# Optimization experiments

Hardware: AMD Instinct MI355X
Metric: run time of the kernel (lower is better)

Reference implementation:

```python
import jax, jax.numpy as jnp
import numpy as np

N_SPECIES = 4; N_BASIS = 128; N_GRAPH = 16; R_MAX = 6.0
NS_NODE, NV_NODE = 32, 16          # node irreps 32x0e + 16x1o
NS_EDGE = 16                       # initial edge irreps 16x0e
NS_OUT, NV_OUT = 16, 8             # output irreps 16x0e + 8x1o
NS_IN = 2 * NS_NODE + NS_EDGE      # 80 concatenated scalars
NV_IN = 2 * NV_NODE                # 32 concatenated vectors
NS_CONV = NS_OUT + NV_OUT          # 24 scalars (16 features + 8 gates)
W_SIZES = [NS_IN * NS_CONV, NS_IN * NV_OUT, NV_IN * NV_OUT, NV_IN * NS_CONV, NV_IN * NV_OUT]
N_NODES, N_EDGES = 8192, 65536
EPS = 1e-5


def gaussian_basis(d, stop, n):
    offsets = jnp.linspace(0.0, stop, n)
    coeff = -0.5 / (offsets[1] - offsets[0]) ** 2
    return jnp.exp(coeff * (d[:, None] - offsets[None, :]) ** 2)


def seg_mean(vals, seg, cnt):
    return jax.ops.segment_sum(vals, seg, num_segments=N_GRAPH) / cnt[:, None]


def setup_inputs():
    key = jax.random.key(0)
    ks = jax.random.split(key, 20)
    rn = lambda k, shape, scale: jax.random.normal(k, shape, jnp.float32) * scale
    inp = {}
    inp["node_fea"] = rn(ks[0], (N_NODES, NS_NODE + 3 * NV_NODE), 1.0)
    d = 0.5 + 5.0 * jax.random.uniform(ks[1], (N_EDGES,), jnp.float32)
    vec = jax.random.normal(ks[2], (N_EDGES, 3), jnp.float32)
    inp["edge_attr"] = jnp.concatenate([d[:, None], vec], axis=1)
    inp["edge_index"] = jax.random.randint(ks[3], (2, N_EDGES), 0, N_NODES)
    inp["x"] = jax.random.randint(ks[4], (N_NODES,), 0, N_SPECIES)
    inp["batch"] = jnp.sort(jax.random.randint(ks[5], (N_NODES,), 0, N_GRAPH))
    inp["w_rh"] = rn(ks[6], (N_BASIS, 64), N_BASIS ** -0.5); inp["b_rh"] = jnp.zeros((64,), jnp.float32)
    inp["w_ro"] = rn(ks[7], (64, sum(W_SIZES)), 64 ** -0.5); inp["b_ro"] = jnp.zeros((sum(W_SIZES),), jnp.float32)
    inp["w_pre"] = rn(ks[8], (NS_EDGE, NS_EDGE), NS_EDGE ** -0.5); inp["b_pre"] = jnp.zeros((NS_EDGE,), jnp.float32)
    inp["w_sc"] = rn(ks[9], (NS_EDGE, N_SPECIES ** 2, NS_OUT), 1.0)
    inp["w_post_s"] = rn(ks[10], (NS_OUT, NS_OUT), NS_OUT ** -0.5); inp["b_post_s"] = jnp.zeros((NS_OUT,), jnp.float32)
    inp["w_post_v"] = rn(ks[11], (NV_OUT, NV_OUT), NV_OUT ** -0.5)
    inp["ln_w_s"] = jnp.ones((NS_OUT,), jnp.float32); inp["ln_b_s"] = jnp.zeros((NS_OUT,), jnp.float32)
    inp["ln_w_v"] = jnp.ones((NV_OUT,), jnp.float32)
    inp["w_skip"] = rn(ks[12], (NS_EDGE, NS_OUT), NS_EDGE ** -0.5)
    inp["w_edge_s"] = rn(ks[13], (NS_OUT, NS_OUT), NS_OUT ** -0.5); inp["b_edge_s"] = jnp.zeros((NS_OUT,), jnp.float32)
    inp["w_edge_v"] = rn(ks[14], (NV_OUT, NV_OUT), NV_OUT ** -0.5)
    return inp


def _forward(node_fea, edge_attr, w_rh, b_rh, w_ro, b_ro, w_pre, b_pre, w_sc,
             w_post_s, b_post_s, w_post_v, ln_w_s, ln_b_s, ln_w_v,
             w_skip, w_edge_s, b_edge_s, w_edge_v, edge_index, x, batch):
    E = edge_index.shape[1]
    idx_i, idx_j = edge_index[0], edge_index[1]
    one_hot = jax.nn.one_hot(N_SPECIES * x[idx_i] + x[idx_j], N_SPECIES ** 2, dtype=node_fea.dtype)
    d, vec = edge_attr[:, 0], edge_attr[:, 1:4]
    u = vec / (jnp.linalg.norm(vec, axis=1, keepdims=True) + 1e-12)
    Y1 = np.sqrt(3.0) * u                                   # l=1 sph harm, component norm; Y0 == 1
    rbf = gaussian_basis(d, R_MAX, N_BASIS)                 # edge_length_embedded
    edge_s0 = gaussian_basis(d, 6.0, NS_EDGE)               # distance_expansion -> initial edge scalars
    # self connection: edge scalars x species-pair one-hot -> output scalars
    sc = jnp.einsum('ei,ej,ijo->eo', edge_s0, one_hot, w_sc) / np.sqrt(NS_EDGE * N_SPECIES ** 2)
    edge_s = edge_s0 @ w_pre + b_pre                        # lin_pre
    # gather node features by edge indices and concat
    nf_i, nf_j = node_fea[idx_i], node_fea[idx_j]
    s_in = jnp.concatenate([nf_i[:, :NS_NODE], nf_j[:, :NS_NODE], edge_s], axis=1)  # [E,80]
    v_in = jnp.concatenate([nf_i[:, NS_NODE:].reshape(E, NV_NODE, 3),
                            nf_j[:, NS_NODE:].reshape(E, NV_NODE, 3)], axis=1)      # [E,32,3]
    # radial MLP -> per-edge tensor-product path weights
    h = jax.nn.silu(rbf @ w_rh + b_rh)
    w_all = h @ w_ro + b_ro                                 # [E, 3840]
    w1, w2, w3, w4, w5 = jnp.split(w_all, np.cumsum(W_SIZES)[:-1].tolist(), axis=1)
    # equivariant tensor-product paths (explicit l<=1 Clebsch-Gordan structure)
    s0 = jnp.einsum('ei,eio->eo', s_in, w1.reshape(E, NS_IN, NS_CONV)) / np.sqrt(NS_IN)            # 0e x 0e -> 0e
    vA = jnp.einsum('ei,eio,ec->eoc', s_in, w2.reshape(E, NS_IN, NV_OUT), Y1) / np.sqrt(NS_IN)     # 0e x 1o -> 1o
    vB = jnp.einsum('eic,eio->eoc', v_in, w3.reshape(E, NV_IN, NV_OUT)) / np.sqrt(NV_IN)           # 1o x 0e -> 1o
    s1 = jnp.einsum('eic,eio,ec->eo', v_in, w4.reshape(E, NV_IN, NS_CONV), Y1) / np.sqrt(3.0 * NV_IN)  # 1o.1o -> 0e
    vC = jnp.einsum('eic,eio->eoc', jnp.cross(v_in, Y1[:, None, :]), w5.reshape(E, NV_IN, NV_OUT)) / np.sqrt(2.0 * NV_IN)  # 1o x 1o -> 1o
    s_conv = s0 + s1                                        # [E,24]
    v_conv = vA + vB + vC                                   # [E,8,3]
    # gate nonlinearity inside conv
    s_out = jax.nn.silu(s_conv[:, :NS_OUT])
    v_out = v_conv * jax.nn.sigmoid(s_conv[:, NS_OUT:])[:, :, None]
    # lin_post then self connection
    s_out = s_out @ w_post_s + b_post_s + sc
    v_out = jnp.einsum('eic,io->eoc', v_out, w_post_v)
    # e3LayerNorm keyed by graph id of source node
    eb = batch[idx_i]
    cnt = jnp.maximum(jax.ops.segment_sum(jnp.ones((E,), s_out.dtype), eb, num_segments=N_GRAPH), 1.0)
    mu = seg_mean(s_out, eb, cnt)
    s_c = s_out - mu[eb]
    rms_s = jnp.sqrt(seg_mean(s_c ** 2, eb, cnt).mean(axis=1, keepdims=True) + EPS)
    s_n = s_c / rms_s[eb] * ln_w_s + ln_b_s
    rms_v = jnp.sqrt((seg_mean((v_out ** 2).sum(-1), eb, cnt) / 3.0).mean(axis=1, keepdims=True) + EPS)
    v_n = v_out / rms_v[eb][:, :, None] * ln_w_v[None, :, None]
    # skip connection from old edge features (scalars only)
    s_n = s_n + edge_s0 @ w_skip
    # final lin_edge
    s_fin = s_n @ w_edge_s + b_edge_s
    v_fin = jnp.einsum('eic,io->eoc', v_n, w_edge_v)
    return jnp.concatenate([s_fin, v_fin.reshape(E, NV_OUT * 3)], axis=1)  # [E,40]


def reference(node_fea, edge_attr, edge_index, x, batch, w_rh, b_rh, w_ro, b_ro,
              w_pre, b_pre, w_sc, w_post_s, b_post_s, w_post_v, ln_w_s, ln_b_s, ln_w_v,
              w_skip, w_edge_s, b_edge_s, w_edge_v):
    return _forward(node_fea, edge_attr, w_rh, b_rh, w_ro, b_ro, w_pre, b_pre, w_sc,
                    w_post_s, b_post_s, w_post_v, ln_w_s, ln_b_s, ln_w_v,
                    w_skip, w_edge_s, b_edge_s, w_edge_v, edge_index, x, batch)
```

## Files before the change

kernel.cpp:

```cpp
#include <hip/hip_runtime.h>

typedef unsigned short u16;
typedef unsigned int u32;
typedef __attribute__((ext_vector_type(8))) _Float16 half8;
typedef __attribute__((ext_vector_type(2))) __fp16 fp16x2;
typedef __attribute__((ext_vector_type(4))) float floatx4;

#define E_TOTAL 65536

__device__ __forceinline__ u32 pk16(float x0, float x1) {
    union { fp16x2 h; u32 u; } c;
    c.h = __builtin_amdgcn_cvt_pkrtz(x0, x1);
    return c.u;
}
union Frag8h { u32 u[4]; half8 v; };


__global__ __launch_bounds__(1024) void k_init(float* __restrict__ ws, int* __restrict__ binv) {
    const int tid = threadIdx.x;
    for (int i = tid; i < 1056; i += 1024) ws[i] = 0.0f;
    if (tid < 64) {
        const int lane = tid;
        const int q = lane >> 4;
        if (lane < 32) binv[lane] = lane;
        half8 bfr;
        #pragma unroll
        for (int j = 0; j < 8; ++j) bfr[j] = (_Float16)(float)(q*8 + j + 1);
        #pragma unroll
        for (int s = 0; s < 32; ++s) {
            const int qa = s >> 3, ja = s & 7;
            half8 afr;
            #pragma unroll
            for (int j = 0; j < 8; ++j) afr[j] = (_Float16)0.0f;
            if (q == qa) afr[ja] = (_Float16)1.0f;
            floatx4 dc = {0.0f, 0.0f, 0.0f, 0.0f};
            dc = __builtin_amdgcn_mfma_f32_16x16x32_f16(afr, bfr, dc, 0, 0, 0);
            if (lane == 0) {
                const int sB = (int)(dc[0] + 0.5f) - 1;
                if (sB >= 0 && sB < 32) binv[sB] = s;
            }
        }
    }
}

__global__ __launch_bounds__(256) void k_edge_heavy(
    const float* __restrict__ node_fea, const float* __restrict__ edge_attr,
    const int* __restrict__ edge_index, const int* __restrict__ xsp,
    const float* __restrict__ w_rh, const float* __restrict__ b_rh,
    const float* __restrict__ w_ro, const float* __restrict__ b_ro,
    const float* __restrict__ w_pre, const float* __restrict__ b_pre,
    const float* __restrict__ w_sc, const float* __restrict__ w_post_s,
    const float* __restrict__ b_post_s, const float* __restrict__ w_post_v,
    const int* __restrict__ binv,
    float* __restrict__ out)
{
    __shared__ __align__(16) float sh_wt[32][130];
    __shared__ float sh_sin[32][80];
    __shared__ float sh_vl[32][3][32];
    __shared__ float sh_acc[32][56];
    __shared__ float sh_y1[32][4];
    __shared__ int   sh_kmap[32];

    u16*   a_rbf = (u16*)&sh_wt[0][0];
    u16*   a_h   = (u16*)((char*)&sh_wt[0][0] + 8192);
    float* es0f  = (float*)((char*)&sh_wt[0][0] + 12288);

    const int tid = threadIdx.x;
    const int ed = tid >> 4, l16 = tid & 15;
    const int lane = tid & 63, w = tid >> 6;
    const int quad = lane >> 4, l15 = lane & 15;
    const int e0 = blockIdx.x * 32 + ed;
    const int e1 = e0 + 16;

    if (tid < 32) sh_kmap[tid] = binv[tid];

    const int ni0 = edge_index[e0], nj0 = edge_index[E_TOTAL + e0];
    const int ni1 = edge_index[e1], nj1 = edge_index[E_TOTAL + e1];
    const float4 ea0 = *(const float4*)(edge_attr + 4*e0);
    const float4 ea1 = *(const float4*)(edge_attr + 4*e1);
    const float d0 = ea0.x, d1 = ea1.x;
    {
        const float invn0 = 1.0f / (sqrtf(ea0.y*ea0.y + ea0.z*ea0.z + ea0.w*ea0.w) + 1e-12f);
        const float invn1 = 1.0f / (sqrtf(ea1.y*ea1.y + ea1.z*ea1.z + ea1.w*ea1.w) + 1e-12f);
        if (l16 == 0) {
            sh_y1[ed][0]    = 1.7320508075688772f * ea0.y * invn0;
            sh_y1[ed][1]    = 1.7320508075688772f * ea0.z * invn0;
            sh_y1[ed][2]    = 1.7320508075688772f * ea0.w * invn0;
            sh_y1[16+ed][0] = 1.7320508075688772f * ea1.y * invn1;
            sh_y1[16+ed][1] = 1.7320508075688772f * ea1.z * invn1;
            sh_y1[16+ed][2] = 1.7320508075688772f * ea1.w * invn1;
        }
    }

    const float C128 = -0.5f * (127.0f/6.0f) * (127.0f/6.0f);
    const float S128 = 6.0f/127.0f;
    {
        Frag8h t0, t1;
        #pragma unroll
        for (int r2 = 0; r2 < 4; ++r2) {
            const int b0i = l16*8 + 2*r2;
            const float u0 = d0 - S128 * (float)b0i;
            const float u1 = d0 - S128 * (float)(b0i + 1);
            const float v0 = d1 - S128 * (float)b0i;
            const float v1 = d1 - S128 * (float)(b0i + 1);
            t0.u[r2] = pk16(expf(C128*u0*u0), expf(C128*u1*u1));
            t1.u[r2] = pk16(expf(C128*v0*v0), expf(C128*v1*v1));
        }
        *(half8*)&a_rbf[(l16*16 + ed)*8]        = t0.v;
        *(half8*)&a_rbf[2048 + (l16*16 + ed)*8] = t1.v;
    }
    {
        const float t0 = d0 - 0.4f * (float)l16;
        const float t1 = d1 - 0.4f * (float)l16;
        es0f[ed*16 + l16]      = expf(-3.125f * t0 * t0);
        es0f[(16+ed)*16 + l16] = expf(-3.125f * t1 * t1);
    }

    const float rs80 = 0.11180339887498949f;
    const float rs32 = 0.17677669529663689f;
    {
        const float* fi = node_fea + (size_t)ni0 * 80;
        const float* fj = node_fea + (size_t)nj0 * 80;
        sh_sin[ed][2*l16+0]    = fi[2*l16+0] * rs80;
        sh_sin[ed][2*l16+1]    = fi[2*l16+1] * rs80;
        sh_sin[ed][32+2*l16+0] = fj[2*l16+0] * rs80;
        sh_sin[ed][32+2*l16+1] = fj[2*l16+1] * rs80;
        #pragma unroll
        for (int c = 0; c < 3; ++c) {
            sh_vl[ed][c][l16]      = fi[32 + 3*l16 + c] * rs32;
            sh_vl[ed][c][16 + l16] = fj[32 + 3*l16 + c] * rs32;
        }
    }
    {
        const float* fi = node_fea + (size_t)ni1 * 80;
        const float* fj = node_fea + (size_t)nj1 * 80;
        sh_sin[16+ed][2*l16+0]    = fi[2*l16+0] * rs80;
        sh_sin[16+ed][2*l16+1]    = fi[2*l16+1] * rs80;
        sh_sin[16+ed][32+2*l16+0] = fj[2*l16+0] * rs80;
        sh_sin[16+ed][32+2*l16+1] = fj[2*l16+1] * rs80;
        #pragma unroll
        for (int c = 0; c < 3; ++c) {
            sh_vl[16+ed][c][l16]      = fi[32 + 3*l16 + c] * rs32;
            sh_vl[16+ed][c][16 + l16] = fj[32 + 3*l16 + c] * rs32;
        }
    }
    for (int s = tid; s < 32*56; s += 256) (&sh_acc[0][0])[s] = 0.0f;
    __syncthreads();

    int km[8];
    u32 voff0[8], voff1[8];
    #pragma unroll
    for (int j = 0; j < 8; ++j) {
        km[j] = sh_kmap[quad*8 + j];
        voff0[j] = (u32)(km[j] * 3840 + l15);
        voff1[j] = voff0[j] + 32u * 3840u;
    }

    float my_sc0, my_sc1;
    {
        const int o = l16;
        float es0v = b_pre[o], sc0 = 0.0f;
        float es1v = b_pre[o], sc1 = 0.0f;
        const int p0 = 4*xsp[ni0] + xsp[nj0];
        const int p1 = 4*xsp[ni1] + xsp[nj1];
        #pragma unroll
        for (int i = 0; i < 16; ++i) {
            const float g0 = es0f[ed*16 + i];
            const float g1 = es0f[(16+ed)*16 + i];
            es0v += g0 * w_pre[i*16 + o];
            es1v += g1 * w_pre[i*16 + o];
            sc0  += g0 * w_sc[(i*16 + p0)*16 + o];
            sc1  += g1 * w_sc[(i*16 + p1)*16 + o];
        }
        sh_sin[ed][64 + o]    = es0v * rs80;
        sh_sin[16+ed][64 + o] = es1v * rs80;
        my_sc0 = sc0 * 0.0625f;
        my_sc1 = sc1 * 0.0625f;
    }

    {
        floatx4 h0 = {0.0f, 0.0f, 0.0f, 0.0f};
        floatx4 h1 = {0.0f, 0.0f, 0.0f, 0.0f};
        #pragma unroll
        for (int kk = 0; kk < 4; ++kk) {
            const half8 ag0 = *(const half8*)&a_rbf[((kk*4 + quad)*16 + l15)*8];
            const half8 ag1 = *(const half8*)&a_rbf[2048 + ((kk*4 + quad)*16 + l15)*8];
            Frag8h bh;
            #pragma unroll
            for (int jj = 0; jj < 4; ++jj) {
                const float x0 = w_rh[(size_t)(kk*32 + km[2*jj+0])*64 + w*16 + l15];
                const float x1 = w_rh[(size_t)(kk*32 + km[2*jj+1])*64 + w*16 + l15];
                bh.u[jj] = pk16(x0, x1);
            }
            h0 = __builtin_amdgcn_mfma_f32_16x16x32_f16(ag0, bh.v, h0, 0, 0, 0);
            h1 = __builtin_amdgcn_mfma_f32_16x16x32_f16(ag1, bh.v, h1, 0, 0, 0);
        }
        const int hn = w*16 + l15;
        const float bb = b_rh[hn];
        const int k8 = hn >> 3, j2 = hn & 7;
        #pragma unroll
        for (int r = 0; r < 4; ++r) {
            const int m = quad*4 + r;
            {
                const float x = h0[r] + bb;
                const float s = x / (1.0f + expf(-x));
                union { _Float16 h; u16 u; } cv; cv.h = (_Float16)s;
                a_h[(k8*16 + m)*8 + j2] = cv.u;
            }
            {
                const float x = h1[r] + bb;
                const float s = x / (1.0f + expf(-x));
                union { _Float16 h; u16 u; } cv; cv.h = (_Float16)s;
                a_h[1024 + (k8*16 + m)*8 + j2] = cv.u;
            }
        }
    }
    __syncthreads();

    const half8 a0g0 = *(const half8*)&a_h[((0*4 + quad)*16 + l15)*8];
    const half8 a1g0 = *(const half8*)&a_h[((1*4 + quad)*16 + l15)*8];
    const half8 a0g1 = *(const half8*)&a_h[1024 + ((0*4 + quad)*16 + l15)*8];
    const half8 a1g1 = *(const half8*)&a_h[1024 + ((1*4 + quad)*16 + l15)*8];

    float pf[32];
    float pbias[2];
    #pragma unroll
    for (int ct = 0; ct < 2; ++ct) {
        const int sgct = __builtin_amdgcn_readfirstlane(w*2 + ct);
        const float* bp = w_ro + sgct*16;
        #pragma unroll
        for (int j = 0; j < 8; ++j) {
            pf[ct*16 + j]     = bp[voff0[j]];
            pf[ct*16 + 8 + j] = bp[voff1[j]];
        }
        pbias[ct] = b_ro[sgct*16 + l15];
    }

    for (int ch = 0; ch < 30; ++ch) {
        const int coff = ch * 128;
        floatx4 acc0[2], acc1[2];
        float bias[2];
        #pragma unroll
        for (int ct = 0; ct < 2; ++ct) {
            Frag8h b0, b1;
            #pragma unroll
            for (int jj = 0; jj < 4; ++jj) {
                b0.u[jj] = pk16(pf[ct*16 + 2*jj],     pf[ct*16 + 2*jj+1]);
                b1.u[jj] = pk16(pf[ct*16 + 8 + 2*jj], pf[ct*16 + 8 + 2*jj+1]);
            }
            floatx4 a = {0.0f, 0.0f, 0.0f, 0.0f};
            a = __builtin_amdgcn_mfma_f32_16x16x32_f16(a0g0, b0.v, a, 0, 0, 0);
            a = __builtin_amdgcn_mfma_f32_16x16x32_f16(a1g0, b1.v, a, 0, 0, 0);
            acc0[ct] = a;
            floatx4 c = {0.0f, 0.0f, 0.0f, 0.0f};
            c = __builtin_amdgcn_mfma_f32_16x16x32_f16(a0g1, b0.v, c, 0, 0, 0);
            c = __builtin_amdgcn_mfma_f32_16x16x32_f16(a1g1, b1.v, c, 0, 0, 0);
            acc1[ct] = c;
            bias[ct] = pbias[ct];
        }
        __syncthreads();
        #pragma unroll
        for (int ct = 0; ct < 2; ++ct) {
            const int col = w*32 + ct*16 + l15;
            #pragma unroll
            for (int r = 0; r < 4; ++r) {
                sh_wt[quad*4 + r][col]      = acc0[ct][r] + bias[ct];
                sh_wt[16 + quad*4 + r][col] = acc1[ct][r] + bias[ct];
            }
        }
        __syncthreads();

        if (ch < 29) {
            #pragma unroll
            for (int ct = 0; ct < 2; ++ct) {
                const int sgct = __builtin_amdgcn_readfirstlane((ch+1)*8 + w*2 + ct);
                const float* bp = w_ro + sgct*16;
                #pragma unroll
                for (int j = 0; j < 8; ++j) {
                    pf[ct*16 + j]     = bp[voff0[j]];
                    pf[ct*16 + 8 + j] = bp[voff1[j]];
                }
                pbias[ct] = b_ro[sgct*16 + l15];
            }
        }

        if (ch < 15) {
            for (int idx = tid; idx < 768; idx += 256) {
                const int eo = idx / 24, o = idx % 24;
                const int i0 = (coff > o) ? (coff - o + 23) / 24 : 0;
                int i1 = (coff + 128 - o + 23) / 24; if (i1 > 80) i1 = 80;
                float a = 0.0f;
                for (int i = i0; i < i1; ++i)
                    a += sh_sin[eo][i] * sh_wt[eo][i*24 + o - coff];
                sh_acc[eo][o] += a;
            }
        } else if (ch < 20) {
            const int ib = (ch - 15) * 16;
            for (int idx = tid; idx < 256; idx += 256) {
                const int eo = idx >> 3, o = idx & 7;
                float a = 0.0f;
                #pragma unroll
                for (int i = 0; i < 16; ++i)
                    a += sh_sin[eo][ib + i] * sh_wt[eo][i*8 + o];
                sh_acc[eo][24 + o] += a;
            }
        } else if (ch < 22) {
            const int ib = (ch - 20) * 16;
            for (int idx = tid; idx < 768; idx += 256) {
                const int eo = idx / 24, rem = idx % 24;
                const int o = rem / 3, cc = rem % 3;
                float a = 0.0f;
                #pragma unroll
                for (int i = 0; i < 16; ++i)
                    a += sh_vl[eo][cc][ib + i] * sh_wt[eo][i*8 + o];
                sh_acc[eo][32 + o*3 + cc] += a;
            }
        } else if (ch < 28) {
            const int rel = coff - 2816;
            for (int idx = tid; idx < 768; idx += 256) {
                const int eo = idx / 24, o = idx % 24;
                const int i0 = (rel > o) ? (rel - o + 23) / 24 : 0;
                int i1 = (rel + 128 - o + 23) / 24; if (i1 > 32) i1 = 32;
                const float Ya = sh_y1[eo][0], Yb = sh_y1[eo][1], Yc = sh_y1[eo][2];
                float a = 0.0f;
                for (int i = i0; i < i1; ++i) {
                    const float qv = sh_vl[eo][0][i]*Ya + sh_vl[eo][1][i]*Yb
                                   + sh_vl[eo][2][i]*Yc;
                    a += qv * sh_wt[eo][i*24 + o - rel];
                }
                sh_acc[eo][o] += a * 0.57735026918962573f;
            }
        } else {
            const int ib = (ch - 28) * 16;
            for (int idx = tid; idx < 768; idx += 256) {
                const int eo = idx / 24, rem = idx % 24;
                const int o = rem / 3, cc = rem % 3;
                const int c1 = (cc < 2) ? cc + 1 : 0;
                const int c2 = (c1 < 2) ? c1 + 1 : 0;
                const float Yp = sh_y1[eo][c2];
                const float Ym = sh_y1[eo][c1];
                float a = 0.0f;
                #pragma unroll
                for (int i = 0; i < 16; ++i)
                    a += (sh_vl[eo][c1][ib+i]*Yp - sh_vl[eo][c2][ib+i]*Ym) * sh_wt[eo][i*8 + o];
                sh_acc[eo][32 + o*3 + cc] += a * 0.70710678118654746f;
            }
        }
    }
    __syncthreads();

    #pragma unroll
    for (int g = 0; g < 2; ++g) {
        const int er = g*16 + ed;
        const int e  = (g == 0) ? e0 : e1;
        const float msc = (g == 0) ? my_sc0 : my_sc1;
        {
            const int o = l16;
            float a = b_post_s[o] + msc;
            #pragma unroll
            for (int i = 0; i < 16; ++i) {
                const float sv = sh_acc[er][i];
                a += (sv / (1.0f + expf(-sv))) * w_post_s[i*16 + o];
            }
            out[(size_t)e*40 + o] = a;
        }
        if (l16 < 8) {
            const int o = l16;
            const float Ya = sh_y1[er][0], Yb = sh_y1[er][1], Yc = sh_y1[er][2];
            float r0 = 0.0f, r1 = 0.0f, r2 = 0.0f;
            #pragma unroll
            for (int i = 0; i < 8; ++i) {
                const float gt = 1.0f / (1.0f + expf(-sh_acc[er][16 + i]));
                const float a2 = sh_acc[er][24 + i];
                const float ww = w_post_v[i*8 + o];
                r0 += (a2*Ya + sh_acc[er][32 + i*3 + 0]) * gt * ww;
                r1 += (a2*Yb + sh_acc[er][32 + i*3 + 1]) * gt * ww;
                r2 += (a2*Yc + sh_acc[er][32 + i*3 + 2]) * gt * ww;
            }
            out[(size_t)e*40 + 16 + o*3 + 0] = r0;
            out[(size_t)e*40 + 16 + o*3 + 1] = r1;
            out[(size_t)e*40 + 16 + o*3 + 2] = r2;
        }
    }
}

__global__ __launch_bounds__(256) void k_stats_partial(
    const float* __restrict__ sv, const int* __restrict__ edge_index,
    const int* __restrict__ batch, float* __restrict__ ws)
{
    __shared__ float bins[768];
    const int tid = threadIdx.x;
    for (int s = tid; s < 768; s += 256) bins[s] = 0.0f;
    __syncthreads();

    const int e = blockIdx.x * 256 + tid;
    const int g = batch[edge_index[e]];
    const float* p = sv + (size_t)e * 40;
    float v[40];
    #pragma unroll
    for (int j = 0; j < 40; ++j) v[j] = p[j];

    float* bg = bins + g * 48;
    #pragma unroll
    for (int chn = 0; chn < 16; ++chn) {
        atomicAdd(&bg[chn],      v[chn]);
        atomicAdd(&bg[16 + chn], v[chn] * v[chn]);
    }
    #pragma unroll
    for (int o = 0; o < 8; ++o) {
        const float a = v[16 + o*3], b = v[16 + o*3 + 1], c = v[16 + o*3 + 2];
        atomicAdd(&bg[32 + o], a*a + b*b + c*c);
    }
    atomicAdd(&bg[40], 1.0f);
    __syncthreads();

    for (int s = tid; s < 768; s += 256) {
        const float x = bins[s];
        if (x != 0.0f) atomicAdd(&ws[s], x);
    }
}

__global__ __launch_bounds__(256) void k_edge_final(
    float* buf, const float* __restrict__ ws,
    const float* __restrict__ edge_attr, const int* __restrict__ edge_index,
    const int* __restrict__ batch,
    const float* __restrict__ ln_w_s, const float* __restrict__ ln_b_s,
    const float* __restrict__ ln_w_v, const float* __restrict__ w_skip,
    const float* __restrict__ w_edge_s, const float* __restrict__ b_edge_s,
    const float* __restrict__ w_edge_v)
{
    __shared__ float sh_mu[16][16];
    __shared__ float sh_is[16], sh_iv[16];
    __shared__ float sh_lws[16], sh_lbs[16], sh_lwv[8];
    __shared__ float sh_skip[16][16], sh_wes[16][16], sh_bes[16], sh_wev[8][8];
    const int tid = threadIdx.x;
    if (tid < 16) {
        const int g = tid;
        float cnt = ws[g*48 + 40]; if (cnt < 1.0f) cnt = 1.0f;
        const float ic = 1.0f / cnt;
        float vs = 0.0f;
        for (int chn = 0; chn < 16; ++chn) {
            const float mu = ws[g*48 + chn] * ic;
            sh_mu[g][chn] = mu;
            vs += ws[g*48 + 16 + chn] * ic - mu * mu;
        }
        if (vs < 0.0f) vs = 0.0f;
        sh_is[g] = 1.0f / sqrtf(vs * (1.0f/16.0f) + 1e-5f);
        float vv = 0.0f;
        for (int o = 0; o < 8; ++o) vv += ws[g*48 + 32 + o];
        vv = vv * ic * (1.0f/3.0f) * (1.0f/8.0f);
        sh_iv[g] = 1.0f / sqrtf(vv + 1e-5f);
    }
    sh_skip[tid >> 4][tid & 15] = w_skip[tid];
    sh_wes[tid >> 4][tid & 15]  = w_edge_s[tid];
    if (tid < 16) {
        sh_lws[tid] = ln_w_s[tid];
        sh_lbs[tid] = ln_b_s[tid];
        sh_bes[tid] = b_edge_s[tid];
    }
    if (tid < 8)  sh_lwv[tid] = ln_w_v[tid];
    if (tid < 64) sh_wev[tid >> 3][tid & 7] = w_edge_v[tid];
    __syncthreads();

    const int e = blockIdx.x * 256 + tid;
    const int g = batch[edge_index[e]];
    const float d = edge_attr[4*e];
    float es0[16];
    #pragma unroll
    for (int b = 0; b < 16; ++b) {
        const float t = d - 0.4f * (float)b;
        es0[b] = expf(-3.125f * t * t);
    }
    float p[40];
    float* pb = buf + (size_t)e * 40;
    #pragma unroll
    for (int j = 0; j < 40; ++j) p[j] = pb[j];

    const float is = sh_is[g];
    float sn[16];
    #pragma unroll
    for (int chn = 0; chn < 16; ++chn)
        sn[chn] = (p[chn] - sh_mu[g][chn]) * is * sh_lws[chn] + sh_lbs[chn];
    #pragma unroll
    for (int b = 0; b < 16; ++b) {
        const float g0 = es0[b];
        #pragma unroll
        for (int chn = 0; chn < 16; ++chn) sn[chn] += g0 * sh_skip[b][chn];
    }
    #pragma unroll
    for (int o = 0; o < 16; ++o) {
        float a = sh_bes[o];
        #pragma unroll
        for (int chn = 0; chn < 16; ++chn) a += sn[chn] * sh_wes[chn][o];
        pb[o] = a;
    }
    const float iv = sh_iv[g];
    float vn[8][3];
    #pragma unroll
    for (int i = 0; i < 8; ++i) {
        const float f = iv * sh_lwv[i];
        vn[i][0] = p[16 + i*3 + 0] * f;
        vn[i][1] = p[16 + i*3 + 1] * f;
        vn[i][2] = p[16 + i*3 + 2] * f;
    }
    #pragma unroll
    for (int o = 0; o < 8; ++o) {
        float r0 = 0.0f, r1 = 0.0f, r2 = 0.0f;
        #pragma unroll
        for (int i = 0; i < 8; ++i) {
            const float w = sh_wev[i][o];
            r0 += vn[i][0] * w; r1 += vn[i][1] * w; r2 += vn[i][2] * w;
        }
        pb[16 + o*3 + 0] = r0;
        pb[16 + o*3 + 1] = r1;
        pb[16 + o*3 + 2] = r2;
    }
}

extern "C" void kernel_launch(void* const* d_in, const int* in_sizes, int n_in,
                              void* d_out, int out_size, void* d_ws, size_t ws_size,
                              hipStream_t stream)
{
    const float* node_fea  = (const float*)d_in[0];
    const float* edge_attr = (const float*)d_in[1];
    const int* edge_index  = (const int*)d_in[2];
    const int* xsp         = (const int*)d_in[3];
    const int* batch       = (const int*)d_in[4];
    const float* w_rh      = (const float*)d_in[5];
    const float* b_rh      = (const float*)d_in[6];
    const float* w_ro      = (const float*)d_in[7];
    const float* b_ro      = (const float*)d_in[8];
    const float* w_pre     = (const float*)d_in[9];
    const float* b_pre     = (const float*)d_in[10];
    const float* w_sc      = (const float*)d_in[11];
    const float* w_post_s  = (const float*)d_in[12];
    const float* b_post_s  = (const float*)d_in[13];
    const float* w_post_v  = (const float*)d_in[14];
    const float* ln_w_s    = (const float*)d_in[15];
    const float* ln_b_s    = (const float*)d_in[16];
    const float* ln_w_v    = (const float*)d_in[17];
    const float* w_skip    = (const float*)d_in[18];
    const float* w_edge_s  = (const float*)d_in[19];
    const float* b_edge_s  = (const float*)d_in[20];
    const float* w_edge_v  = (const float*)d_in[21];

    float* ws   = (float*)d_ws;
    int*   binv = (int*)(ws + 1056);
    float* out  = (float*)d_out;

    k_init<<<1, 1024, 0, stream>>>(ws, binv);
    k_edge_heavy<<<2048, 256, 0, stream>>>(node_fea, edge_attr, edge_index, xsp,
        w_rh, b_rh, w_ro, b_ro, w_pre, b_pre, w_sc, w_post_s, b_post_s, w_post_v,
        binv, out);
    k_stats_partial<<<256, 256, 0, stream>>>(out, edge_index, batch, ws);
    k_edge_final<<<256, 256, 0, stream>>>(out, ws, edge_attr, edge_index,
        batch, ln_w_s, ln_b_s, ln_w_v, w_skip, w_edge_s, b_edge_s, w_edge_v);
}
```

Baseline: 411.1 us.

## Fuse per-graph stats into edge kernel and double-buffer weight tile

```diff
diff --git a/kernel.cpp b/kernel.cpp
--- a/kernel.cpp
+++ b/kernel.cpp
@@ -51,19 +51,20 @@
     const float* __restrict__ w_pre, const float* __restrict__ b_pre,
     const float* __restrict__ w_sc, const float* __restrict__ w_post_s,
     const float* __restrict__ b_post_s, const float* __restrict__ w_post_v,
-    const int* __restrict__ binv,
+    const int* __restrict__ binv, const int* __restrict__ batch,
+    float* __restrict__ ws_stats,
     float* __restrict__ out)
 {
-    __shared__ __align__(16) float sh_wt[32][130];
+    __shared__ __align__(16) float sh_wt[2][32][130];
     __shared__ float sh_sin[32][80];
     __shared__ float sh_vl[32][3][32];
     __shared__ float sh_acc[32][56];
     __shared__ float sh_y1[32][4];
     __shared__ int   sh_kmap[32];
 
-    u16*   a_rbf = (u16*)&sh_wt[0][0];
-    u16*   a_h   = (u16*)((char*)&sh_wt[0][0] + 8192);
-    float* es0f  = (float*)((char*)&sh_wt[0][0] + 12288);
+    u16*   a_rbf = (u16*)&sh_wt[0][0][0];
+    u16*   a_h   = (u16*)((char*)&sh_wt[0][0][0] + 8192);
+    float* es0f  = (float*)((char*)&sh_wt[0][0][0] + 12288);
 
     const int tid = threadIdx.x;
     const int ed = tid >> 4, l16 = tid & 15;
@@ -221,6 +222,7 @@
     const half8 a1g0 = *(const half8*)&a_h[((1*4 + quad)*16 + l15)*8];
     const half8 a0g1 = *(const half8*)&a_h[1024 + ((0*4 + quad)*16 + l15)*8];
     const half8 a1g1 = *(const half8*)&a_h[1024 + ((1*4 + quad)*16 + l15)*8];
+    __syncthreads();
 
     float pf[32];
     float pbias[2];
@@ -238,6 +240,7 @@
 
     for (int ch = 0; ch < 30; ++ch) {
         const int coff = ch * 128;
+        float (*wt)[130] = sh_wt[ch & 1];
         floatx4 acc0[2], acc1[2];
         float bias[2];
         #pragma unroll
@@ -258,14 +261,13 @@
             acc1[ct] = c;
             bias[ct] = pbias[ct];
         }
-        __syncthreads();
         #pragma unroll
         for (int ct = 0; ct < 2; ++ct) {
             const int col = w*32 + ct*16 + l15;
             #pragma unroll
             for (int r = 0; r < 4; ++r) {
-                sh_wt[quad*4 + r][col]      = acc0[ct][r] + bias[ct];
-                sh_wt[16 + quad*4 + r][col] = acc1[ct][r] + bias[ct];
+                wt[quad*4 + r][col]      = acc0[ct][r] + bias[ct];
+                wt[16 + quad*4 + r][col] = acc1[ct][r] + bias[ct];
             }
         }
         __syncthreads();
@@ -291,7 +293,7 @@
                 int i1 = (coff + 128 - o + 23) / 24; if (i1 > 80) i1 = 80;
                 float a = 0.0f;
                 for (int i = i0; i < i1; ++i)
-                    a += sh_sin[eo][i] * sh_wt[eo][i*24 + o - coff];
+                    a += sh_sin[eo][i] * wt[eo][i*24 + o - coff];
                 sh_acc[eo][o] += a;
             }
         } else if (ch < 20) {
@@ -301,7 +303,7 @@
                 float a = 0.0f;
                 #pragma unroll
                 for (int i = 0; i < 16; ++i)
-                    a += sh_sin[eo][ib + i] * sh_wt[eo][i*8 + o];
+                    a += sh_sin[eo][ib + i] * wt[eo][i*8 + o];
                 sh_acc[eo][24 + o] += a;
             }
         } else if (ch < 22) {
@@ -312,7 +314,7 @@
                 float a = 0.0f;
                 #pragma unroll
                 for (int i = 0; i < 16; ++i)
-                    a += sh_vl[eo][cc][ib + i] * sh_wt[eo][i*8 + o];
+                    a += sh_vl[eo][cc][ib + i] * wt[eo][i*8 + o];
                 sh_acc[eo][32 + o*3 + cc] += a;
             }
         } else if (ch < 28) {
@@ -326,7 +328,7 @@
                 for (int i = i0; i < i1; ++i) {
                     const float qv = sh_vl[eo][0][i]*Ya + sh_vl[eo][1][i]*Yb
                                    + sh_vl[eo][2][i]*Yc;
-                    a += qv * sh_wt[eo][i*24 + o - rel];
+                    a += qv * wt[eo][i*24 + o - rel];
                 }
                 sh_acc[eo][o] += a * 0.57735026918962573f;
             }
@@ -342,17 +344,24 @@
                 float a = 0.0f;
                 #pragma unroll
                 for (int i = 0; i < 16; ++i)
-                    a += (sh_vl[eo][c1][ib+i]*Yp - sh_vl[eo][c2][ib+i]*Ym) * sh_wt[eo][i*8 + o];
+                    a += (sh_vl[eo][c1][ib+i]*Yp - sh_vl[eo][c2][ib+i]*Ym) * wt[eo][i*8 + o];
                 sh_acc[eo][32 + o*3 + cc] += a * 0.70710678118654746f;
             }
         }
     }
     __syncthreads();
 
+    float* bins = &sh_wt[0][0][0];
+    for (int s = tid; s < 768; s += 256) bins[s] = 0.0f;
+    __syncthreads();
+
+    const int gi0 = batch[ni0];
+    const int gi1 = batch[ni1];
     #pragma unroll
     for (int g = 0; g < 2; ++g) {
         const int er = g*16 + ed;
         const int e  = (g == 0) ? e0 : e1;
+        const int gi = (g == 0) ? gi0 : gi1;
         const float msc = (g == 0) ? my_sc0 : my_sc1;
         {
             const int o = l16;
@@ -363,6 +372,9 @@
                 a += (sv / (1.0f + expf(-sv))) * w_post_s[i*16 + o];
             }
             out[(size_t)e*40 + o] = a;
+            atomicAdd(&bins[gi*48 + o], a);
+            atomicAdd(&bins[gi*48 + 16 + o], a*a);
+            if (o == 0) atomicAdd(&bins[gi*48 + 40], 1.0f);
         }
         if (l16 < 8) {
             const int o = l16;
@@ -380,43 +392,13 @@
             out[(size_t)e*40 + 16 + o*3 + 0] = r0;
             out[(size_t)e*40 + 16 + o*3 + 1] = r1;
             out[(size_t)e*40 + 16 + o*3 + 2] = r2;
-        }
-    }
-}
-
-__global__ __launch_bounds__(256) void k_stats_partial(
-    const float* __restrict__ sv, const int* __restrict__ edge_index,
-    const int* __restrict__ batch, float* __restrict__ ws)
-{
-    __shared__ float bins[768];
-    const int tid = threadIdx.x;
-    for (int s = tid; s < 768; s += 256) bins[s] = 0.0f;
-    __syncthreads();
-
-    const int e = blockIdx.x * 256 + tid;
-    const int g = batch[edge_index[e]];
-    const float* p = sv + (size_t)e * 40;
-    float v[40];
-    #pragma unroll
-    for (int j = 0; j < 40; ++j) v[j] = p[j];
-
-    float* bg = bins + g * 48;
-    #pragma unroll
-    for (int chn = 0; chn < 16; ++chn) {
-        atomicAdd(&bg[chn],      v[chn]);
-        atomicAdd(&bg[16 + chn], v[chn] * v[chn]);
-    }
-    #pragma unroll
-    for (int o = 0; o < 8; ++o) {
-        const float a = v[16 + o*3], b = v[16 + o*3 + 1], c = v[16 + o*3 + 2];
-        atomicAdd(&bg[32 + o], a*a + b*b + c*c);
-    }
-    atomicAdd(&bg[40], 1.0f);
-    __syncthreads();
-
+            atomicAdd(&bins[gi*48 + 32 + o], r0*r0 + r1*r1 + r2*r2);
+        }
+    }
+    __syncthreads();
     for (int s = tid; s < 768; s += 256) {
         const float x = bins[s];
-        if (x != 0.0f) atomicAdd(&ws[s], x);
+        if (x != 0.0f) atomicAdd(&ws_stats[s], x);
     }
 }
 
@@ -551,8 +533,7 @@
     k_init<<<1, 1024, 0, stream>>>(ws, binv);
     k_edge_heavy<<<2048, 256, 0, stream>>>(node_fea, edge_attr, edge_index, xsp,
         w_rh, b_rh, w_ro, b_ro, w_pre, b_pre, w_sc, w_post_s, b_post_s, w_post_v,
-        binv, out);
-    k_stats_partial<<<256, 256, 0, stream>>>(out, edge_index, batch, ws);
+        binv, batch, ws, out);
     k_edge_final<<<256, 256, 0, stream>>>(out, ws, edge_attr, edge_index,
         batch, ln_w_s, ln_b_s, ln_w_v, w_skip, w_edge_s, b_edge_s, w_edge_v);
 }
```

Result: no change. 406.9 us (-1.0%).
